# Performance work log

Hardware: AMD Instinct MI355X
Metric: run time of the kernel (lower is better)

## Reference

```python
import jax, jax.numpy as jnp
import numpy as np
import math

B, D, K = 256, 128, 4096
OUTPUT_SIZE = 1281167
T = 0.07


def setup_inputs() -> dict:
    key = jax.random.key(0)
    k1, k2, k3, k4 = jax.random.split(key, 4)
    x = jax.random.normal(k1, (B, D), dtype=jnp.float32)
    y = jax.random.randint(k2, (B,), 0, OUTPUT_SIZE, dtype=jnp.int64)
    idx = jax.random.randint(k3, (B, K + 1), 0, OUTPUT_SIZE, dtype=jnp.int64)
    stdv = 1.0 / math.sqrt(D / 3.0)
    memory = jax.random.uniform(k4, (OUTPUT_SIZE, D), dtype=jnp.float32,
                                minval=-stdv, maxval=stdv)
    return {"x": x, "y": y, "idx": idx, "memory": memory}


def reference(x, y, idx, memory):
    outputSize = memory.shape[0]
    # first column of idx is overwritten with the positive index y
    idx = idx.at[:, 0].set(y)
    # gather K+1 rows per sample from the memory bank: (B, K+1, D)
    weight = memory[idx]
    # batched dot product: (B, K+1)
    logits = jnp.einsum('bkd,bd->bk', weight, x) / T
    e = jnp.exp(logits)
    # Z is set on first call from the batch statistics (params[2] == -1 path)
    Z = e.mean() * outputSize
    out = e / Z
    return out
```

## Files before the change

kernel.cpp:

```cpp
#include <hip/hip_runtime.h>


constexpr int       kB          = 256;
constexpr int       kKp1        = 4097;
constexpr long long kOutRows    = 1281167LL;
constexpr int       kSplits     = 8;
constexpr int       kMainBlocks = kB * kSplits;
constexpr int       kThreads    = 256;
constexpr float     kInvT       = 1.0f / 0.07f;

__device__ __forceinline__ float dot4(float4 a, float4 b) {
    return a.x * b.x + a.y * b.y + a.z * b.z + a.w * b.w;
}

__global__ __launch_bounds__(kThreads) void nce_main(
    const float* __restrict__ x, const int* __restrict__ y,
    const int* __restrict__ idx, const float* __restrict__ memory,
    float* __restrict__ out, float* __restrict__ blksum)
{
    const int b     = blockIdx.x >> 3;
    const int chunk = blockIdx.x & 7;
    const int tid   = threadIdx.x;
    const int wave  = tid >> 6;
    const int lane  = tid & 63;
    const int dlane = lane & 31;
    const int g     = wave * 2 + (lane >> 5);

    const float4  xv   = reinterpret_cast<const float4*>(x)[b * 32 + dlane];
    const float4* m4   = reinterpret_cast<const float4*>(memory);
    const int*    idxb = idx + (size_t)b * kKp1;
    float*        outb = out + (size_t)b * kKp1;

    const int k0 = chunk * 512;
    const int k1 = (chunk == 7) ? kKp1 : k0 + 512;

    float acc = 0.0f;
    int kb = k0 + g * 4;

    if (kb + 4 <= k1) {
        int r0 = (kb == 0) ? y[b] : idxb[kb];
        int r1 = idxb[kb + 1], r2 = idxb[kb + 2], r3 = idxb[kb + 3];
        while (true) {
            const float4 a0 = m4[(size_t)r0 * 32 + dlane];
            const float4 a1 = m4[(size_t)r1 * 32 + dlane];
            const float4 a2 = m4[(size_t)r2 * 32 + dlane];
            const float4 a3 = m4[(size_t)r3 * 32 + dlane];

            const int knext = kb + 32;
            const bool more = (knext + 4 <= k1);
            int s0, s1, s2, s3;
            if (more) {
                s0 = idxb[knext];     s1 = idxb[knext + 1];
                s2 = idxb[knext + 2]; s3 = idxb[knext + 3];
            }

            float d0 = dot4(a0, xv), d1 = dot4(a1, xv);
            float d2 = dot4(a2, xv), d3 = dot4(a3, xv);
            #pragma unroll
            for (int m = 16; m >= 1; m >>= 1) {
                d0 += __shfl_xor(d0, m, 64);
                d1 += __shfl_xor(d1, m, 64);
                d2 += __shfl_xor(d2, m, 64);
                d3 += __shfl_xor(d3, m, 64);
            }
            if (dlane == 0) {
                const float e0 = __expf(d0 * kInvT);
                const float e1 = __expf(d1 * kInvT);
                const float e2 = __expf(d2 * kInvT);
                const float e3 = __expf(d3 * kInvT);
                outb[kb]     = e0;  acc += e0;
                outb[kb + 1] = e1;  acc += e1;
                outb[kb + 2] = e2;  acc += e2;
                outb[kb + 3] = e3;  acc += e3;
            }
            if (!more) { kb = knext; break; }
            kb = knext;
            r0 = s0; r1 = s1; r2 = s2; r3 = s3;
        }
    }

    for (int k = kb; k < k1; ++k) {
        const int row = idxb[k];
        const float4 a = m4[(size_t)row * 32 + dlane];
        float d = dot4(a, xv);
        #pragma unroll
        for (int m = 16; m >= 1; m >>= 1)
            d += __shfl_xor(d, m, 64);
        if (dlane == 0) {
            const float e = __expf(d * kInvT);
            outb[k] = e;  acc += e;
        }
    }

    #pragma unroll
    for (int m = 32; m >= 1; m >>= 1)
        acc += __shfl_xor(acc, m, 64);
    __shared__ float red[kThreads / 64];
    if (lane == 0) red[wave] = acc;
    __syncthreads();
    if (tid == 0)
        blksum[blockIdx.x] = red[0] + red[1] + red[2] + red[3];
}

__global__ __launch_bounds__(256) void nce_norm(
    float4* __restrict__ out4, const float* __restrict__ blksum, int n4)
{
    float s = 0.0f;
    for (int i = threadIdx.x; i < kMainBlocks; i += 256) s += blksum[i];
    #pragma unroll
    for (int m = 32; m >= 1; m >>= 1)
        s += __shfl_xor(s, m, 64);
    __shared__ float red[4];
    if ((threadIdx.x & 63) == 0) red[threadIdx.x >> 6] = s;
    __syncthreads();
    const float tot = red[0] + red[1] + red[2] + red[3];
    const float sc = ((float)(kB * kKp1) / (float)kOutRows) / tot;

    int i = blockIdx.x * blockDim.x + threadIdx.x;
    const int stride = gridDim.x * blockDim.x;
    for (; i < n4; i += stride) {
        float4 v = out4[i];
        v.x *= sc; v.y *= sc; v.z *= sc; v.w *= sc;
        out4[i] = v;
    }
}

extern "C" void kernel_launch(void* const* d_in, const int* in_sizes, int n_in,
                              void* d_out, int out_size, void* d_ws, size_t ws_size,
                              hipStream_t stream) {
    const float* x      = (const float*)d_in[0];
    const int*   y      = (const int*)d_in[1];
    const int*   idx    = (const int*)d_in[2];
    const float* memory = (const float*)d_in[3];
    float*       out    = (float*)d_out;
    float*       blksum = (float*)d_ws;

    hipLaunchKernelGGL(nce_main, dim3(kMainBlocks), dim3(kThreads), 0, stream,
                       x, y, idx, memory, out, blksum);
    hipLaunchKernelGGL(nce_norm, dim3(1024), dim3(256), 0, stream,
                       (float4*)d_out, blksum, out_size / 4);
}
```

Before: 93.09 us.

## Gather eight rows per half-wave and use butterfly transpose-reduce for dot products

Each 32-lane group now gathers eight memory rows per iteration instead of four, giving more loads in flight. The eight dot products are reduced with a recursive-halving exchange, so each shuffle step carries useful data for several rows and the shuffle count drops from 20 to 9 per eight rows. Eight lanes per group then write outputs instead of one. The prefetch of the next index set is removed, and the last column is handled as a special case, which may expose index-load latency.

```diff
diff --git a/kernel.cpp b/kernel.cpp
--- a/kernel.cpp
+++ b/kernel.cpp
@@ -30,57 +30,59 @@
     const float4* m4   = reinterpret_cast<const float4*>(memory);
     const int*    idxb = idx + (size_t)b * kKp1;
     float*        outb = out + (size_t)b * kKp1;
+    const int     ypos = y[b];
 
     const int k0 = chunk * 512;
-    const int k1 = (chunk == 7) ? kKp1 : k0 + 512;
+    float acc = 0.0f;
 
-    float acc = 0.0f;
-    int kb = k0 + g * 4;
+    const bool storer = (dlane & 3) == 0;
+    const int  jmap   = ((dlane >> 2) & 1) * 4 + ((dlane >> 3) & 1) * 2 +
+                        ((dlane >> 4) & 1);
 
-    if (kb + 4 <= k1) {
-        int r0 = (kb == 0) ? y[b] : idxb[kb];
-        int r1 = idxb[kb + 1], r2 = idxb[kb + 2], r3 = idxb[kb + 3];
-        while (true) {
-            const float4 a0 = m4[(size_t)r0 * 32 + dlane];
-            const float4 a1 = m4[(size_t)r1 * 32 + dlane];
-            const float4 a2 = m4[(size_t)r2 * 32 + dlane];
-            const float4 a3 = m4[(size_t)r3 * 32 + dlane];
+    int kb = k0 + g * 8;
+    #pragma unroll 1
+    for (int it = 0; it < 8; ++it, kb += 64) {
+        const int r0 = (kb == 0) ? ypos : idxb[kb];
+        const int r1 = idxb[kb + 1], r2 = idxb[kb + 2], r3 = idxb[kb + 3];
+        const int r4 = idxb[kb + 4], r5 = idxb[kb + 5];
+        const int r6 = idxb[kb + 6], r7 = idxb[kb + 7];
 
-            const int knext = kb + 32;
-            const bool more = (knext + 4 <= k1);
-            int s0, s1, s2, s3;
-            if (more) {
-                s0 = idxb[knext];     s1 = idxb[knext + 1];
-                s2 = idxb[knext + 2]; s3 = idxb[knext + 3];
-            }
+        const float4 a0 = m4[(size_t)r0 * 32 + dlane];
+        const float4 a1 = m4[(size_t)r1 * 32 + dlane];
+        const float4 a2 = m4[(size_t)r2 * 32 + dlane];
+        const float4 a3 = m4[(size_t)r3 * 32 + dlane];
+        const float4 a4 = m4[(size_t)r4 * 32 + dlane];
+        const float4 a5 = m4[(size_t)r5 * 32 + dlane];
+        const float4 a6 = m4[(size_t)r6 * 32 + dlane];
+        const float4 a7 = m4[(size_t)r7 * 32 + dlane];
 
-            float d0 = dot4(a0, xv), d1 = dot4(a1, xv);
-            float d2 = dot4(a2, xv), d3 = dot4(a3, xv);
-            #pragma unroll
-            for (int m = 16; m >= 1; m >>= 1) {
-                d0 += __shfl_xor(d0, m, 64);
-                d1 += __shfl_xor(d1, m, 64);
-                d2 += __shfl_xor(d2, m, 64);
-                d3 += __shfl_xor(d3, m, 64);
-            }
-            if (dlane == 0) {
-                const float e0 = __expf(d0 * kInvT);
-                const float e1 = __expf(d1 * kInvT);
-                const float e2 = __expf(d2 * kInvT);
-                const float e3 = __expf(d3 * kInvT);
-                outb[kb]     = e0;  acc += e0;
-                outb[kb + 1] = e1;  acc += e1;
-                outb[kb + 2] = e2;  acc += e2;
-                outb[kb + 3] = e3;  acc += e3;
-            }
-            if (!more) { kb = knext; break; }
-            kb = knext;
-            r0 = s0; r1 = s1; r2 = s2; r3 = s3;
+        const float d0 = dot4(a0, xv), d1 = dot4(a1, xv);
+        const float d2 = dot4(a2, xv), d3 = dot4(a3, xv);
+        const float d4 = dot4(a4, xv), d5 = dot4(a5, xv);
+        const float d6 = dot4(a6, xv), d7 = dot4(a7, xv);
+
+        const bool h16 = (dlane & 16) != 0;
+        float r01 = (h16 ? d1 : d0) + __shfl_xor(h16 ? d0 : d1, 16, 64);
+        float r23 = (h16 ? d3 : d2) + __shfl_xor(h16 ? d2 : d3, 16, 64);
+        float r45 = (h16 ? d5 : d4) + __shfl_xor(h16 ? d4 : d5, 16, 64);
+        float r67 = (h16 ? d7 : d6) + __shfl_xor(h16 ? d6 : d7, 16, 64);
+        const bool h8 = (dlane & 8) != 0;
+        float r03 = (h8 ? r23 : r01) + __shfl_xor(h8 ? r01 : r23, 8, 64);
+        float r47 = (h8 ? r67 : r45) + __shfl_xor(h8 ? r45 : r67, 8, 64);
+        const bool h4 = (dlane & 4) != 0;
+        float r = (h4 ? r47 : r03) + __shfl_xor(h4 ? r03 : r47, 4, 64);
+        r += __shfl_xor(r, 2, 64);
+        r += __shfl_xor(r, 1, 64);
+
+        const float e = __expf(r * kInvT);
+        if (storer) {
+            outb[kb + jmap] = e;
+            acc += e;
         }
     }
 
-    for (int k = kb; k < k1; ++k) {
-        const int row = idxb[k];
+    if (chunk == 7 && g == 0) {
+        const int row = idxb[4096];
         const float4 a = m4[(size_t)row * 32 + dlane];
         float d = dot4(a, xv);
         #pragma unroll
@@ -88,7 +90,7 @@
             d += __shfl_xor(d, m, 64);
         if (dlane == 0) {
             const float e = __expf(d * kInvT);
-            outb[k] = e;  acc += e;
+            outb[4096] = e;  acc += e;
         }
     }
 
```

Result: no change. 91.83 us (-1.4%).
